# Optimization experiments

Measured on AMD Instinct MI355X. Metric: run time of the kernel, lower is better.

The kernel has to match this reference:

```python
import jax, jax.numpy as jnp
import numpy as np

B, C, L = 32, 512, 4096
H, K = 8, 3            # heads, kernel_size
D = C // H             # head dim
G = 32                 # GroupNorm groups
PAD = (K - 1) // 2
EPS = 1e-5
NEG = -1e30


def setup_inputs() -> dict:
    key = jax.random.key(0)
    ks = jax.random.split(key, 7)
    s = 0.02
    return {
        "x": jax.random.normal(ks[0], (B, C, L), dtype=jnp.float32),
        "gamma": jnp.ones((C,), dtype=jnp.float32),
        "beta": jnp.zeros((C,), dtype=jnp.float32),
        "W_k": jax.random.normal(ks[1], (C, H * D), dtype=jnp.float32) * s,
        "W_v": jax.random.normal(ks[2], (C, H * D), dtype=jnp.float32) * s,
        "W_o": jax.random.normal(ks[3], (H * D, C), dtype=jnp.float32) * s,
        "q": jax.random.normal(ks[4], (H, D), dtype=jnp.float32) * s,     # learned queries (QnA)
        "rpe": jax.random.normal(ks[5], (H, K), dtype=jnp.float32) * s,   # relative-position bias
    }


def _group_norm(x, gamma, beta):
    # x: (B, C, L); normalize over (C//G, L) within each of G groups
    b, c, l = x.shape
    xg = x.reshape(b, G, (c // G) * l)
    mu = jnp.mean(xg, axis=-1, keepdims=True)
    var = jnp.var(xg, axis=-1, keepdims=True)
    xn = ((xg - mu) * jax.lax.rsqrt(var + EPS)).reshape(b, c, l)
    return xn * gamma[None, :, None] + beta[None, :, None]


def reference(x, gamma, beta, W_k, W_v, W_o, q, rpe):
    h = _group_norm(x, gamma, beta)                     # (B, C, L)
    ht = jnp.transpose(h, (0, 2, 1))                    # (B, L, C)
    k = (ht @ W_k).reshape(B, L, H, D)                  # (B, L, H, D)
    v = (ht @ W_v).reshape(B, L, H, D)

    scale = 1.0 / np.sqrt(D).astype(np.float32)
    logits = jnp.einsum('blhd,hd->blh', k, q) * scale   # (B, L, H)

    # sliding windows of size K (zero-padded; -inf logits at boundaries)
    lp = jnp.pad(logits, ((0, 0), (PAD, PAD), (0, 0)), constant_values=NEG)
    lwin = jnp.stack([lp[:, j:j + L] for j in range(K)], axis=2)      # (B, L, K, H)
    lwin = lwin + jnp.transpose(rpe)[None, None]                       # rpe: (H,K)->(K,H)
    attn = jax.nn.softmax(lwin, axis=2)                                # (B, L, K, H)

    vp = jnp.pad(v, ((0, 0), (PAD, PAD), (0, 0), (0, 0)))
    vwin = jnp.stack([vp[:, j:j + L] for j in range(K)], axis=2)       # (B, L, K, H, D)
    o = jnp.einsum('blkh,blkhd->blhd', attn, vwin).reshape(B, L, H * D)

    out = (o @ W_o)                                      # (B, L, C)
    return x + jnp.transpose(out, (0, 2, 1))             # residual, (B, C, L)
```

## Files before the change

### kernel.cpp

```cpp
#include <hip/hip_runtime.h>

#define Bb 32
#define Cc 512
#define Ll 4096
#define Hh 8
#define Dd 64
#define Gg 32
#define BLt (Bb * Ll)
#define NKV 520
#define NKVPAD 640

typedef __attribute__((ext_vector_type(4))) float f32x4;
typedef __attribute__((ext_vector_type(8))) short short8;
typedef __attribute__((ext_vector_type(4))) short s16x4;
typedef __attribute__((ext_vector_type(4))) int int4v;

union U16 { int4v v; short s[8]; };

__device__ __forceinline__ float bf2f(short s) {
    unsigned u = ((unsigned)(unsigned short)s) << 16;
    float f; __builtin_memcpy(&f, &u, 4); return f;
}
__device__ __forceinline__ short f2bf(float f) {
    unsigned u; __builtin_memcpy(&u, &f, 4);
    u = (u + 0x7FFFu + ((u >> 16) & 1u)) >> 16;
    return (short)u;
}

__device__ __forceinline__ int kpack(int k) {
    int blk = k >> 5, r = k & 31;
    return blk * 32 + ((r & 15) >> 2) * 8 + ((r >> 4) << 2) + (r & 3);
}

__device__ __forceinline__ int swz_off(int row, int inner) {
    return row * 128 + (inner ^ ((row & 7) << 4));
}

__device__ __forceinline__ void gload16(const short* g, short* l) {
    __builtin_amdgcn_global_load_lds((const __attribute__((address_space(1))) unsigned int*)g,
                                     (__attribute__((address_space(3))) unsigned int*)l,
                                     16, 0, 0);
}
__device__ __forceinline__ void gload16f(const float* g, float* l) {
    __builtin_amdgcn_global_load_lds((const __attribute__((address_space(1))) unsigned int*)g,
                                     (__attribute__((address_space(3))) unsigned int*)l,
                                     16, 0, 0);
}

#define BAR() __builtin_amdgcn_s_barrier()
#define SFENCE() __builtin_amdgcn_sched_barrier(0)

__global__ void k_prep(const float* __restrict__ Wk, const float* __restrict__ Wv,
                       const float* __restrict__ Wo, const float* __restrict__ q,
                       short* __restrict__ Wct, short* __restrict__ Wot, int packWo)
{
    int bid = blockIdx.x, t = threadIdx.x;
    if (bid < NKVPAD) {
        int n = bid;
        if (n < 512) {
            for (int k = t; k < 512; k += 64)
                Wct[n * 512 + kpack(k)] = f2bf(Wv[k * 512 + n]);
        } else if (n < NKV) {
            int h = n - 512;
            for (int k = t; k < 512; k += 64) {
                float acc = 0.f;
                for (int d = 0; d < 64; ++d)
                    acc += Wk[k * 512 + h * 64 + d] * q[h * 64 + d];
                Wct[n * 512 + kpack(k)] = f2bf(acc * 0.125f);
            }
        } else {
            for (int k = t; k < 512; k += 64) Wct[n * 512 + kpack(k)] = 0;
        }
    } else {
        int c = bid - NKVPAD;
        for (int k = t; k < 512; k += 64)
            Wot[c * 512 + (packWo ? kpack(k) : k)] = f2bf(Wo[k * 512 + c]);
    }
}

__global__ void k_stats(const float* __restrict__ x, float* __restrict__ stats)
{
    int bg = blockIdx.x;
    const float* p = x + (size_t)bg * 65536;
    int t = threadIdx.x;
    float s = 0.f, ss = 0.f;
    for (int i = t * 4; i < 65536; i += 1024) {
        f32x4 v = *(const f32x4*)(p + i);
        s  += v[0] + v[1] + v[2] + v[3];
        ss += v[0]*v[0] + v[1]*v[1] + v[2]*v[2] + v[3]*v[3];
    }
    for (int o = 32; o > 0; o >>= 1) { s += __shfl_down(s, o); ss += __shfl_down(ss, o); }
    __shared__ float red[8];
    int lane = t & 63, w = t >> 6;
    if (lane == 0) { red[w] = s; red[4 + w] = ss; }
    __syncthreads();
    if (t == 0) {
        float S  = red[0] + red[1] + red[2] + red[3];
        float SS = red[4] + red[5] + red[6] + red[7];
        float mean = S * (1.0f / 65536.0f);
        float var  = SS * (1.0f / 65536.0f) - mean * mean;
        stats[bg * 2]     = mean;
        stats[bg * 2 + 1] = rsqrtf(var + 1e-5f);
    }
}

__global__ void k_norm_t(const float* __restrict__ x, const float* __restrict__ gamma,
                         const float* __restrict__ beta, const float* __restrict__ stats,
                         short* __restrict__ hT)
{
    __shared__ float tile[64 * 65];
    int b = blockIdx.z, c0 = blockIdx.y * 64, l0 = blockIdx.x * 64;
    int t = threadIdx.x;
    int lq = t & 15, cq = t >> 4;
    #pragma unroll
    for (int p = 0; p < 4; ++p) {
        int cl = cq + p * 16;
        int c = c0 + cl;
        float mean = stats[(b * 32 + (c >> 4)) * 2];
        float rstd = stats[(b * 32 + (c >> 4)) * 2 + 1];
        float a  = rstd * gamma[c];
        float bb = beta[c] - mean * a;
        f32x4 v = *(const f32x4*)(x + ((size_t)b << 21) + ((size_t)c << 12) + l0 + lq * 4);
        #pragma unroll
        for (int j = 0; j < 4; ++j) tile[cl * 65 + lq * 4 + j] = v[j] * a + bb;
    }
    __syncthreads();
    int ll = t >> 2, cq4 = t & 3;
    int bl = b * Ll + l0 + ll;
    short hbuf[16];
    #pragma unroll
    for (int j = 0; j < 16; ++j) hbuf[j] = f2bf(tile[(cq4 * 16 + j) * 65 + ll]);
    short* dst = hT + (size_t)bl * 512 + ((c0 >> 5) + (cq4 >> 1)) * 32 + ((cq4 & 1) << 2);
    #pragma unroll
    for (int jj = 0; jj < 4; ++jj) {
        s16x4 v4 = { hbuf[jj*4+0], hbuf[jj*4+1], hbuf[jj*4+2], hbuf[jj*4+3] };
        *(s16x4*)(dst + jj * 8) = v4;
    }
}

__launch_bounds__(256, 2)
__global__ void k_gemm1f(const short* __restrict__ A, const short* __restrict__ Bw,
                         short* __restrict__ vbuf, short* __restrict__ lbuf)
{
    __shared__ short sA[2][8192];
    __shared__ short sB[2][8192];
    __shared__ short wqlds[8192];
    const int t = threadIdx.x;
    const int nwg = 1024;
    const int bid = blockIdx.x;
    const int work = (bid & 7) * (nwg >> 3) + (bid >> 3);
    const int ntile = work & 3;
    const int n0 = ntile * 128;
    const int mbase = (work >> 2) * 512;

    const int lane = t & 63, wid = t >> 6;
    const int wm = wid >> 1, wn = wid & 1;
    const int g = lane >> 4, ln = lane & 15;

    {
        int row = t >> 5;
        int cp = (t & 31) * 2;
        int4v v0 = *(const int4v*)(Bw + (size_t)(512 + row) * 512 + cp * 8);
        int4v v1 = *(const int4v*)(Bw + (size_t)(512 + row) * 512 + cp * 8 + 8);
        *(int4v*)((char*)wqlds + row * 1024 + ((cp * 16) ^ ((row & 7) << 4))) = v0;
        *(int4v*)((char*)wqlds + row * 1024 + (((cp + 1) * 16) ^ ((row & 7) << 4))) = v1;
        int4v z = {0, 0, 0, 0};
        int row2 = 8 + (t >> 5);
        *(int4v*)((char*)wqlds + row2 * 1024 + ((cp * 16) ^ ((row2 & 7) << 4))) = z;
        *(int4v*)((char*)wqlds + row2 * 1024 + (((cp + 1) * 16) ^ ((row2 & 7) << 4))) = z;
    }
    asm volatile("s_waitcnt vmcnt(0) lgkmcnt(0)" ::: "memory");
    BAR(); SFENCE();

    const int srow = wid * 8 + (lane >> 3);
    const int sinner = (((lane & 7) ^ ((lane >> 3) & 7)) << 3);
    const short* gAs = A  + (size_t)(mbase + srow) * 512 + sinner;
    const short* gBs = Bw + (size_t)(n0 + srow) * 512 + sinner;

    f32x4 acc[4][4] = {};
    f32x4 accq[4] = {};

    auto stage = [&](int kt, int buf) {
        size_t offA = (size_t)(kt >> 3) * 65536 + (size_t)(kt & 7) * 64;
        size_t offB = (size_t)(kt & 7) * 64;
        #pragma unroll
        for (int gq = 0; gq < 4; ++gq) {
            gload16(gAs + (size_t)gq * 32 * 512 + offA, &sA[buf][gq * 2048 + wid * 512]);
            gload16(gBs + (size_t)gq * 32 * 512 + offB, &sB[buf][gq * 2048 + wid * 512]);
        }
    };
    auto compute = [&](int buf, int kk) {
        #pragma unroll
        for (int ks = 0; ks < 2; ++ks) {
            short8 af[4], bfr[4], bq;
            #pragma unroll
            for (int i = 0; i < 4; ++i) {
                af[i]  = *(const short8*)((const char*)&sA[buf][0] + swz_off(wm * 64 + i * 16 + ln, ks * 64 + g * 16));
                bfr[i] = *(const short8*)((const char*)&sB[buf][0] + swz_off(wn * 64 + i * 16 + ln, ks * 64 + g * 16));
            }
            bq = *(const short8*)((const char*)wqlds + ln * 1024 +
                                  ((kk * 128 + ks * 64 + g * 16) ^ ((ln & 7) << 4)));
            #pragma unroll
            for (int mi = 0; mi < 4; ++mi)
                #pragma unroll
                for (int ni = 0; ni < 4; ++ni)
                    acc[mi][ni] = __builtin_amdgcn_mfma_f32_16x16x32_bf16(af[mi], bfr[ni], acc[mi][ni], 0, 0, 0);
            #pragma unroll
            for (int mi = 0; mi < 4; ++mi)
                accq[mi] = __builtin_amdgcn_mfma_f32_16x16x32_bf16(af[mi], bq, accq[mi], 0, 0, 0);
        }
    };

    stage(0, 0); stage(1, 1);
    #pragma unroll 1
    for (int s = 0; s < 32; ++s) {
        if (s == 31)           asm volatile("s_waitcnt vmcnt(0)"  ::: "memory");
        else if ((s & 7) == 0 && s) asm volatile("s_waitcnt vmcnt(16)" ::: "memory");
        else                   asm volatile("s_waitcnt vmcnt(8)"  ::: "memory");
        BAR(); SFENCE();
        compute(s & 1, s & 7);
        SFENCE();
        if ((s & 7) == 7) {
            BAR();
            int m0 = mbase + (s >> 3) * 128;
            {
                short* scrW = &sB[s & 1][0] + wid * 2048;
                const int blkq = (lane & 7) >> 2, jq = lane & 3;
                #pragma unroll
                for (int p = 0; p < 2; ++p) {
                    #pragma unroll
                    for (int mh = 0; mh < 2; ++mh)
                        #pragma unroll
                        for (int ni = 0; ni < 4; ++ni)
                            #pragma unroll
                            for (int i = 0; i < 4; ++i)
                                scrW[(mh * 16 + g * 4 + i) * 64 + ni * 16 + ln] = f2bf(acc[p * 2 + mh][ni][i]);
                    asm volatile("s_waitcnt lgkmcnt(0)" ::: "memory"); SFENCE();
                    #pragma unroll
                    for (int it = 0; it < 4; ++it) {
                        int mrl = it * 8 + (lane >> 3);
                        const short* bp = scrW + mrl * 64 + blkq * 32;
                        s16x4 lo = *(const s16x4*)(bp + 4 * jq);
                        s16x4 hi = *(const s16x4*)(bp + 16 + 4 * jq);
                        union { int4v v; s16x4 h[2]; } ov;
                        ov.h[0] = lo; ov.h[1] = hi;
                        int m = m0 + wm * 64 + p * 32 + mrl;
                        int nc = n0 + wn * 64 + blkq * 32 + jq * 8;
                        *(int4v*)(vbuf + (size_t)m * 512 + nc) = ov.v;
                    }
                    asm volatile("s_waitcnt lgkmcnt(0)" ::: "memory"); SFENCE();
                }
            }
            if (ntile == 0 && wn == 0 && ln < 8) {
                #pragma unroll
                for (int mi = 0; mi < 4; ++mi)
                    #pragma unroll
                    for (int i = 0; i < 4; ++i) {
                        int m = m0 + wm * 64 + mi * 16 + g * 4 + i;
                        lbuf[(size_t)m * 8 + ln] = f2bf(accq[mi][i]);
                    }
            }
            #pragma unroll
            for (int mi = 0; mi < 4; ++mi) {
                #pragma unroll
                for (int ni = 0; ni < 4; ++ni)
                    acc[mi][ni] = (f32x4){0.f, 0.f, 0.f, 0.f};
                accq[mi] = (f32x4){0.f, 0.f, 0.f, 0.f};
            }
        }
        if (s < 30) { BAR(); stage(s + 2, s & 1); SFENCE(); }
    }
}

__global__ void k_attnw2(const short* __restrict__ lbuf, const float* __restrict__ rpe,
                         float* __restrict__ attnW)
{
    int tid = blockIdx.x * 256 + threadIdx.x;
    int bl = tid >> 3, h = tid & 7;
    int l = bl & (Ll - 1);
    float lg0 = (l > 0)      ? bf2f(lbuf[(size_t)(bl - 1) * 8 + h]) + rpe[h * 3 + 0] : -1e30f;
    float lg1 =                bf2f(lbuf[(size_t)bl * 8 + h])       + rpe[h * 3 + 1];
    float lg2 = (l < Ll - 1) ? bf2f(lbuf[(size_t)(bl + 1) * 8 + h]) + rpe[h * 3 + 2] : -1e30f;
    float m = fmaxf(lg1, fmaxf(lg0, lg2));
    float e0 = (l > 0)      ? __expf(lg0 - m) : 0.f;
    float e1 =                __expf(lg1 - m);
    float e2 = (l < Ll - 1) ? __expf(lg2 - m) : 0.f;
    float inv = 1.0f / (e0 + e1 + e2);
    f32x4 w = { e0 * inv, e1 * inv, e2 * inv, 0.0f };
    *(f32x4*)(attnW + (size_t)bl * 32 + h * 4) = w;
}

__launch_bounds__(256, 2)
__global__ void k_gemm2f(const short* __restrict__ Wot, const short* __restrict__ vbuf,
                         const float* __restrict__ attnW, const float* __restrict__ x,
                         float* __restrict__ out)
{
    __shared__ short sA[2][8192];
    __shared__ short sBc[2][8192];
    __shared__ float wlds[4096];
    const int t = threadIdx.x;
    const int nwg = 1024;
    const int bid = blockIdx.x;
    const int work = (bid & 7) * (nwg >> 3) + (bid >> 3);
    const int n0 = work * 128;

    const int lane = t & 63, wid = t >> 6;
    const int wm = wid >> 1, wn = wid & 1;
    const int g = lane >> 4, ln = lane & 15;

    const int srow = wid * 8 + (lane >> 3);
    const int sinner = (((lane & 7) ^ ((lane >> 3) & 7)) << 3);
    const short* gAs = Wot + (size_t)srow * 512 + sinner;

    unsigned ovm[4], ov0[4], ovp[4];
    #pragma unroll
    for (int q2 = 0; q2 < 4; ++q2) {
        int r = n0 + srow + 32 * q2;
        int l = r & (Ll - 1);
        int rm = (l == 0) ? r : r - 1;
        int rp = (l == Ll - 1) ? r : r + 1;
        ov0[q2] = (unsigned)r  * 1024u + (unsigned)sinner * 2u;
        ovm[q2] = (unsigned)rm * 1024u + (unsigned)sinner * 2u;
        ovp[q2] = (unsigned)rp * 1024u + (unsigned)sinner * 2u;
    }
    const char* vb = (const char*)vbuf;

    const int r4 = lane >> 4, lcm = (lane & 15) * 4;
    const int ngE = n0 + wn * 64 + lcm;
    const size_t rowbase = ((size_t)(ngE >> 12) << 21) + (size_t)(ngE & (Ll - 1));
    const float* xrow = x + rowbase;
    float* outrow = out + rowbase;

    f32x4 acc[4][4] = {};
    U16 Rm[4], R0[4], Rp[4];

    auto stageA = [&](int s, int buf) {
        size_t off = (size_t)(s >> 3) * 65536 + (size_t)(s & 7) * 64;
        #pragma unroll
        for (int gq = 0; gq < 4; ++gq)
            gload16(gAs + (size_t)gq * 32 * 512 + off, &sA[buf][gq * 2048 + wid * 512]);
    };
    auto loadR = [&](int s1) {
        unsigned off = (unsigned)(s1 & 7) * 128u;
        #pragma unroll
        for (int q2 = 0; q2 < 4; ++q2) {
            Rm[q2].v = *(const int4v*)(vb + ovm[q2] + off);
            R0[q2].v = *(const int4v*)(vb + ov0[q2] + off);
            Rp[q2].v = *(const int4v*)(vb + ovp[q2] + off);
        }
    };
    auto combineStep = [&](int s1, int buf) {
        int h = s1 & 7;
        #pragma unroll
        for (int q2 = 0; q2 < 4; ++q2) {
            int r = srow + 32 * q2;
            f32x4 w = *(const f32x4*)&wlds[r * 32 + ((h ^ (r & 7)) << 2)];
            U16 cm;
            #pragma unroll
            for (int j = 0; j < 8; ++j) {
                float o = w[0] * bf2f(Rm[q2].s[j]) + w[1] * bf2f(R0[q2].s[j])
                        + w[2] * bf2f(Rp[q2].s[j]);
                cm.s[j] = f2bf(o);
            }
            *(int4v*)((char*)&sBc[buf][0] + q2 * 4096 + wid * 1024 + lane * 16) = cm.v;
        }
    };
    auto compute = [&](int buf) {
        #pragma unroll
        for (int ks = 0; ks < 2; ++ks) {
            short8 af[4], bfr[4];
            #pragma unroll
            for (int i = 0; i < 4; ++i) {
                af[i]  = *(const short8*)((const char*)&sA[buf][0] + swz_off(wm * 64 + i * 16 + ln, ks * 64 + g * 16));
                bfr[i] = *(const short8*)((const char*)&sBc[buf][0] + swz_off(wn * 64 + i * 16 + ln, ks * 64 + g * 16));
            }
            #pragma unroll
            for (int mi = 0; mi < 4; ++mi)
                #pragma unroll
                for (int ni = 0; ni < 4; ++ni)
                    acc[mi][ni] = __builtin_amdgcn_mfma_f32_16x16x32_bf16(af[mi], bfr[ni], acc[mi][ni], 0, 0, 0);
        }
    };
    auto epilogue = [&](int s) {
        BAR();
        float* scr = (float*)((char*)&sA[s & 1][0] + wid * 4096);
        int m0c = (s >> 3) * 128;
        #pragma unroll
        for (int p = 0; p < 4; ++p) {
            #pragma unroll
            for (int ni = 0; ni < 4; ++ni)
                #pragma unroll
                for (int i = 0; i < 4; ++i) {
                    int r = g * 4 + i;
                    int col = (ni * 16 + ln) ^ ((((r & 3) ^ (r >> 2)) & 3) << 4);
                    scr[r * 64 + col] = acc[p][ni][i];
                }
            asm volatile("s_waitcnt lgkmcnt(0)" ::: "memory"); SFENCE();
            #pragma unroll
            for (int j = 0; j < 4; ++j) {
                int rr = r4 + 4 * j;
                int cst = lcm ^ ((((rr & 3) ^ (rr >> 2)) & 3) << 4);
                f32x4 sv = *(const f32x4*)&scr[rr * 64 + cst];
                int c = m0c + wm * 64 + p * 16 + rr;
                f32x4 xv = *(const f32x4*)(xrow + ((size_t)c << 12));
                *(f32x4*)(outrow + ((size_t)c << 12)) = xv + sv;
            }
            asm volatile("s_waitcnt lgkmcnt(0)" ::: "memory"); SFENCE();
        }
        #pragma unroll
        for (int mi = 0; mi < 4; ++mi)
            #pragma unroll
            for (int ni = 0; ni < 4; ++ni)
                acc[mi][ni] = (f32x4){0.f, 0.f, 0.f, 0.f};
    };

    stageA(0, 0); stageA(1, 1);
    {
        const float* wsrc = attnW + (size_t)n0 * 32;
        int rr = lane >> 3, hl = lane & 7;
        #pragma unroll
        for (int j = 0; j < 4; ++j) {
            int row = (wid * 4 + j) * 8 + rr;
            gload16f(wsrc + row * 32 + ((hl ^ (row & 7)) << 2), &wlds[(wid * 4 + j) * 256]);
        }
    }
    loadR(0); SFENCE();
    asm volatile("s_waitcnt vmcnt(0)" ::: "memory");
    BAR(); SFENCE();
    combineStep(0, 0);
    asm volatile("s_waitcnt lgkmcnt(0)" ::: "memory"); SFENCE();
    loadR(1); SFENCE();

    #pragma unroll 1
    for (int s = 0; s < 32; ++s) {
        if (s == 0 || s == 31)       asm volatile("s_waitcnt vmcnt(0)"  ::: "memory");
        else if ((s & 7) == 0)       asm volatile("s_waitcnt vmcnt(36)" ::: "memory");
        else                         asm volatile("s_waitcnt vmcnt(4)"  ::: "memory");
        BAR(); SFENCE();
        if (s < 31) {
            combineStep(s + 1, (s + 1) & 1);
            SFENCE();
            if (s < 30) { loadR(s + 2); SFENCE(); }
        }
        compute(s & 1);
        asm volatile("s_waitcnt lgkmcnt(0)" ::: "memory"); SFENCE();
        if ((s & 7) == 7) epilogue(s);
        if (s < 30) { BAR(); stageA(s + 2, s & 1); SFENCE(); }
    }
}

__launch_bounds__(256, 2)
__global__ void k_gemm1_fb(const short* __restrict__ A, const short* __restrict__ Bw,
                           short* __restrict__ kv)
{
    __shared__ short sA[2][8192];
    __shared__ short sB[2][8192];
    const int t = threadIdx.x;
    const int m0 = blockIdx.y * 128;
    const int n0 = blockIdx.x * 128;
    const int lane = t & 63, wid = t >> 6;
    const int wm = wid >> 1, wn = wid & 1;
    const int g = lane >> 4, ln = lane & 15;

    const int srow = wid * 8 + (lane >> 3);
    const int sinner = (((lane & 7) ^ ((lane >> 3) & 7)) << 3);
    const short* gAs = A  + (size_t)(m0 + srow) * 512 + sinner;
    const short* gBs = Bw + (size_t)(n0 + srow) * 512 + sinner;

    f32x4 acc[4][4] = {};

    auto stage = [&](int kt, int buf) {
        #pragma unroll
        for (int gq = 0; gq < 4; ++gq) {
            gload16(gAs + (size_t)gq * 32 * 512 + kt * 64, &sA[buf][gq * 2048 + wid * 512]);
            gload16(gBs + (size_t)gq * 32 * 512 + kt * 64, &sB[buf][gq * 2048 + wid * 512]);
        }
    };
    auto compute = [&](int buf) {
        #pragma unroll
        for (int ks = 0; ks < 2; ++ks) {
            short8 af[4], bfr[4];
            #pragma unroll
            for (int i = 0; i < 4; ++i) {
                af[i]  = *(const short8*)((const char*)&sA[buf][0] + swz_off(wm * 64 + i * 16 + ln, ks * 64 + g * 16));
                bfr[i] = *(const short8*)((const char*)&sB[buf][0] + swz_off(wn * 64 + i * 16 + ln, ks * 64 + g * 16));
            }
            #pragma unroll
            for (int mi = 0; mi < 4; ++mi)
                #pragma unroll
                for (int ni = 0; ni < 4; ++ni)
                    acc[mi][ni] = __builtin_amdgcn_mfma_f32_16x16x32_bf16(af[mi], bfr[ni], acc[mi][ni], 0, 0, 0);
        }
    };

    stage(0, 0);
    __syncthreads();
    #pragma unroll 1
    for (int kt = 0; kt < 8; ++kt) {
        if (kt < 7) stage(kt + 1, (kt + 1) & 1);
        compute(kt & 1);
        __syncthreads();
    }

    #pragma unroll
    for (int mi = 0; mi < 4; ++mi)
        #pragma unroll
        for (int ni = 0; ni < 4; ++ni) {
            int n = n0 + wn * 64 + ni * 16 + ln;
            if (n < NKV) {
                #pragma unroll
                for (int i = 0; i < 4; ++i) {
                    int m = m0 + wm * 64 + mi * 16 + g * 4 + i;
                    kv[(size_t)m * NKV + n] = f2bf(acc[mi][ni][i]);
                }
            }
        }
}

__global__ void k_attnw(const short* __restrict__ kv, const float* __restrict__ rpe,
                        float* __restrict__ attnW)
{
    int tid = blockIdx.x * 256 + threadIdx.x;
    int bl = tid >> 3, h = tid & 7;
    int l = bl & (Ll - 1);
    float lg[3];
    #pragma unroll
    for (int j = 0; j < 3; ++j) {
        bool valid = (j == 1) || (j == 0 && l > 0) || (j == 2 && l < Ll - 1);
        lg[j] = valid ? (bf2f(kv[(size_t)(bl + j - 1) * NKV + 512 + h]) + rpe[h * 3 + j])
                      : -1e30f;
    }
    float m = fmaxf(lg[0], fmaxf(lg[1], lg[2]));
    float e0 = __expf(lg[0] - m), e1 = __expf(lg[1] - m), e2 = __expf(lg[2] - m);
    float inv = 1.0f / (e0 + e1 + e2);
    f32x4 w = { e0 * inv, e1 * inv, e2 * inv, 0.0f };
    *(f32x4*)(attnW + (size_t)bl * 32 + h * 4) = w;
}

__launch_bounds__(256, 2)
__global__ void k_gemm2_fused(const short* __restrict__ Wot, const short* __restrict__ kv,
                              const float* __restrict__ attnW, const float* __restrict__ x,
                              float* __restrict__ out)
{
    __shared__ short sA[2][8192];
    __shared__ short sB[2][8192];
    const int t = threadIdx.x;
    const int m0 = blockIdx.x * 128;
    const int n0 = blockIdx.y * 128;
    const int lane = t & 63, wid = t >> 6;
    const int wm = wid >> 1, wn = wid & 1;
    const int g = lane >> 4, ln = lane & 15;
    const int sr = t >> 1, ksh = t & 1;

    const short* gA = Wot + (size_t)(m0 + sr) * 512 + ksh * 32;
    const int nrow = n0 + sr;
    const int lpos = nrow & (Ll - 1);
    const int nm1 = (lpos == 0) ? nrow : nrow - 1;
    const int np1 = (lpos == Ll - 1) ? nrow : nrow + 1;
    const short* gV0 = kv + (size_t)nrow * NKV + ksh * 32;
    const short* gVm = kv + (size_t)nm1  * NKV + ksh * 32;
    const short* gVp = kv + (size_t)np1  * NKV + ksh * 32;
    const float* gW = attnW + (size_t)nrow * 32;

    f32x4 acc[4][4] = {};
    U16 ra[4], rbm[4], rb0[4], rbp[4];
    f32x4 wv;

    auto load_tile = [&](int kt) {
        #pragma unroll
        for (int qq = 0; qq < 4; ++qq) {
            ra[qq].v  = *(const int4v*)(gA  + kt * 64 + qq * 8);
            rbm[qq].v = *(const int4v*)(gVm + kt * 64 + qq * 8);
            rb0[qq].v = *(const int4v*)(gV0 + kt * 64 + qq * 8);
            rbp[qq].v = *(const int4v*)(gVp + kt * 64 + qq * 8);
        }
        wv = *(const f32x4*)(gW + kt * 4);
    };
    auto write_tile = [&](int buf) {
        short ob[32];
        #pragma unroll
        for (int qq = 0; qq < 4; ++qq)
            #pragma unroll
            for (int j = 0; j < 8; ++j) {
                float o = wv[0] * bf2f(rbm[qq].s[j]) + wv[1] * bf2f(rb0[qq].s[j])
                        + wv[2] * bf2f(rbp[qq].s[j]);
                ob[qq * 8 + j] = f2bf(o);
            }
        #pragma unroll
        for (int f = 0; f < 4; ++f) {
            U16 wa, wb;
            #pragma unroll
            for (int j = 0; j < 4; ++j) {
                wa.s[j]     = ra[f >> 1].s[(f & 1) * 4 + j];
                wa.s[4 + j] = ra[2 + (f >> 1)].s[(f & 1) * 4 + j];
                wb.s[j]     = ob[4 * f + j];
                wb.s[4 + j] = ob[16 + 4 * f + j];
            }
            int off = swz_off(sr, ksh * 64 + f * 16);
            *(int4v*)((char*)&sA[buf][0] + off) = wa.v;
            *(int4v*)((char*)&sB[buf][0] + off) = wb.v;
        }
    };
    auto compute = [&](int buf) {
        #pragma unroll
        for (int ks = 0; ks < 2; ++ks) {
            short8 af[4], bfr[4];
            #pragma unroll
            for (int i = 0; i < 4; ++i) {
                af[i]  = *(const short8*)((const char*)&sA[buf][0] + swz_off(wm * 64 + i * 16 + ln, ks * 64 + g * 16));
                bfr[i] = *(const short8*)((const char*)&sB[buf][0] + swz_off(wn * 64 + i * 16 + ln, ks * 64 + g * 16));
            }
            #pragma unroll
            for (int mi = 0; mi < 4; ++mi)
                #pragma unroll
                for (int ni = 0; ni < 4; ++ni)
                    acc[mi][ni] = __builtin_amdgcn_mfma_f32_16x16x32_bf16(af[mi], bfr[ni], acc[mi][ni], 0, 0, 0);
        }
    };

    load_tile(0); write_tile(0); __syncthreads();
    #pragma unroll 1
    for (int kt = 0; kt < 8; ++kt) {
        if (kt < 7) load_tile(kt + 1);
        compute(kt & 1);
        if (kt < 7) write_tile((kt + 1) & 1);
        __syncthreads();
    }

    #pragma unroll
    for (int mi = 0; mi < 4; ++mi)
        #pragma unroll
        for (int ni = 0; ni < 4; ++ni)
            #pragma unroll
            for (int i = 0; i < 4; ++i) {
                int c = m0 + wm * 64 + mi * 16 + g * 4 + i;
                int ng = n0 + wn * 64 + ni * 16 + ln;
                int b = ng >> 12, l = ng & (Ll - 1);
                size_t off = ((size_t)b << 21) | ((size_t)c << 12) | (size_t)l;
                out[off] = x[off] + acc[mi][ni][i];
            }
}

extern "C" void kernel_launch(void* const* d_in, const int* in_sizes, int n_in,
                              void* d_out, int out_size, void* d_ws, size_t ws_size,
                              hipStream_t stream)
{
    const float* x     = (const float*)d_in[0];
    const float* gamma = (const float*)d_in[1];
    const float* beta  = (const float*)d_in[2];
    const float* Wk    = (const float*)d_in[3];
    const float* Wv    = (const float*)d_in[4];
    const float* Wo    = (const float*)d_in[5];
    const float* q     = (const float*)d_in[6];
    const float* rpe   = (const float*)d_in[7];
    float* out = (float*)d_out;
    char* ws = (char*)d_ws;

    const size_t MB128 = 134217728ull;
    const size_t MAIN_WS = MB128 * 2 + 655360 + 524288 + 2097152 + 8192;

    if (ws_size >= MAIN_WS) {
        float* attnW = (float*)(ws);
        short* vbuf  = (short*)(ws + MB128);
        short* Wct   = (short*)(ws + 2 * MB128);
        short* Wot   = (short*)(ws + 2 * MB128 + 655360);
        short* lbuf  = (short*)(ws + 2 * MB128 + 655360 + 524288);
        float* stats = (float*)(ws + 2 * MB128 + 655360 + 524288 + 2097152);
        short* hT    = (short*)d_out;

        k_prep<<<1152, 64, 0, stream>>>(Wk, Wv, Wo, q, Wct, Wot, 1);
        k_stats<<<1024, 256, 0, stream>>>(x, stats);
        k_norm_t<<<dim3(64, 8, 32), 256, 0, stream>>>(x, gamma, beta, stats, hT);
        k_gemm1f<<<1024, 256, 0, stream>>>(hT, Wct, vbuf, lbuf);
        k_attnw2<<<4096, 256, 0, stream>>>(lbuf, rpe, attnW);
        k_gemm2f<<<1024, 256, 0, stream>>>(Wot, vbuf, attnW, x, out);
    } else {
        short* Wct   = (short*)(ws + 0);
        short* Wot   = (short*)(ws + 655360);
        float* stats = (float*)(ws + 1179648);
        float* attnW = (float*)(ws + 1187840);
        short* kv    = (short*)(ws + 17965056);
        short* hT    = (short*)d_out;

        k_prep<<<1152, 64, 0, stream>>>(Wk, Wv, Wo, q, Wct, Wot, 0);
        k_stats<<<1024, 256, 0, stream>>>(x, stats);
        k_norm_t<<<dim3(64, 8, 32), 256, 0, stream>>>(x, gamma, beta, stats, hT);
        k_gemm1_fb<<<dim3(5, 1024), 256, 0, stream>>>(hT, Wct, kv);
        k_attnw<<<4096, 256, 0, stream>>>(kv, rpe, attnW);
        k_gemm2_fused<<<dim3(4, 1024), 256, 0, stream>>>(Wot, kv, attnW, x, out);
    }
}
```

Measured before the change: 509.8 us.

## Stage V tiles into LDS once and combine sliding window from shared memory

Replaces the per-thread loads of three neighbouring V rows (previous, current, next) from global memory with a single async global-to-LDS staging of each V tile. The tile goes into a triple-buffered LDS array, and the window combine reads the neighbour rows from LDS. Only the two tile-boundary halo rows are fetched separately from global memory. The attention weights are now loaded directly from global memory per step instead of being staged in LDS. This removes the threefold redundant global V traffic, but it adds an extra barrier inside the combine step and keeps the existing vmcnt wait counts, which were tuned for the old load mix.

```diff
diff --git a/kernel.cpp b/kernel.cpp
--- a/kernel.cpp
+++ b/kernel.cpp
@@ -37,11 +37,6 @@
 }
 
 __device__ __forceinline__ void gload16(const short* g, short* l) {
-    __builtin_amdgcn_global_load_lds((const __attribute__((address_space(1))) unsigned int*)g,
-                                     (__attribute__((address_space(3))) unsigned int*)l,
-                                     16, 0, 0);
-}
-__device__ __forceinline__ void gload16f(const float* g, float* l) {
     __builtin_amdgcn_global_load_lds((const __attribute__((address_space(1))) unsigned int*)g,
                                      (__attribute__((address_space(3))) unsigned int*)l,
                                      16, 0, 0);
@@ -296,8 +291,7 @@
                          float* __restrict__ out)
 {
     __shared__ short sA[2][8192];
-    __shared__ short sBc[2][8192];
-    __shared__ float wlds[4096];
+    __shared__ short rawV[3][8192];
     const int t = threadIdx.x;
     const int nwg = 1024;
     const int bid = blockIdx.x;
@@ -309,21 +303,21 @@
     const int g = lane >> 4, ln = lane & 15;
 
     const int srow = wid * 8 + (lane >> 3);
-    const int sinner = (((lane & 7) ^ ((lane >> 3) & 7)) << 3);
-    const short* gAs = Wot + (size_t)srow * 512 + sinner;
-
-    unsigned ovm[4], ov0[4], ovp[4];
-    #pragma unroll
-    for (int q2 = 0; q2 < 4; ++q2) {
-        int r = n0 + srow + 32 * q2;
-        int l = r & (Ll - 1);
-        int rm = (l == 0) ? r : r - 1;
-        int rp = (l == Ll - 1) ? r : r + 1;
-        ov0[q2] = (unsigned)r  * 1024u + (unsigned)sinner * 2u;
-        ovm[q2] = (unsigned)rm * 1024u + (unsigned)sinner * 2u;
-        ovp[q2] = (unsigned)rp * 1024u + (unsigned)sinner * 2u;
-    }
-    const char* vb = (const char*)vbuf;
+    const int gch = lane & 7;
+    const int sinner = ((gch ^ (srow & 7)) << 3);
+    const short* gAs = Wot  + (size_t)srow * 512 + sinner;
+    const short* gVs = vbuf + (size_t)(n0 + srow) * 512 + sinner;
+
+    const int s_own = (gch ^ (srow & 7)) << 4;
+    const int s_rm  = (gch ^ ((srow - 1) & 7)) << 4;
+    const int s_rp  = (gch ^ ((srow + 1) & 7)) << 4;
+
+    const int rbnd = (srow == 0) ? ((n0 == 0) ? 0 : n0 - 1)
+                   : ((srow == 31) ? ((n0 + 128 >= BLt) ? BLt - 1 : n0 + 128)
+                                   : n0 + srow);
+    const short* gBnd = vbuf + (size_t)rbnd * 512 + gch * 8;
+
+    const float* gW = attnW + (size_t)(n0 + srow) * 32;
 
     const int r4 = lane >> 4, lcm = (lane & 15) * 4;
     const int ngE = n0 + wn * 64 + lcm;
@@ -332,7 +326,8 @@
     float* outrow = out + rowbase;
 
     f32x4 acc[4][4] = {};
-    U16 Rm[4], R0[4], Rp[4];
+    f32x4 wq[4];
+    U16 bnd;
 
     auto stageA = [&](int s, int buf) {
         size_t off = (size_t)(s >> 3) * 65536 + (size_t)(s & 7) * 64;
@@ -340,39 +335,57 @@
         for (int gq = 0; gq < 4; ++gq)
             gload16(gAs + (size_t)gq * 32 * 512 + off, &sA[buf][gq * 2048 + wid * 512]);
     };
-    auto loadR = [&](int s1) {
-        unsigned off = (unsigned)(s1 & 7) * 128u;
-        #pragma unroll
-        for (int q2 = 0; q2 < 4; ++q2) {
-            Rm[q2].v = *(const int4v*)(vb + ovm[q2] + off);
-            R0[q2].v = *(const int4v*)(vb + ov0[q2] + off);
-            Rp[q2].v = *(const int4v*)(vb + ovp[q2] + off);
-        }
-    };
-    auto combineStep = [&](int s1, int buf) {
+    auto stageV = [&](int s1) {
+        int b = s1 % 3;
+        size_t off = (size_t)(s1 & 7) * 64;
+        #pragma unroll
+        for (int gq = 0; gq < 4; ++gq)
+            gload16(gVs + (size_t)gq * 32 * 512 + off, &rawV[b][gq * 2048 + wid * 512]);
+    };
+    auto loadWB = [&](int s1) {
         int h = s1 & 7;
+        #pragma unroll
+        for (int q2 = 0; q2 < 4; ++q2)
+            wq[q2] = *(const f32x4*)(gW + q2 * 32 * 32 + h * 4);
+        bnd.v = *(const int4v*)(gBnd + (size_t)h * 64);
+    };
+    auto combine = [&](int s1) {
+        int b = s1 % 3;
+        const char* base = (const char*)&rawV[b][0];
+        U16 vm[4], v0[4], vp[4];
         #pragma unroll
         for (int q2 = 0; q2 < 4; ++q2) {
             int r = srow + 32 * q2;
-            f32x4 w = *(const f32x4*)&wlds[r * 32 + ((h ^ (r & 7)) << 2)];
+            v0[q2].v = *(const int4v*)(base + r * 128 + s_own);
+            vm[q2].v = *(const int4v*)(base + ((r - 1) & 127) * 128 + s_rm);
+            vp[q2].v = *(const int4v*)(base + ((r + 1) & 127) * 128 + s_rp);
+        }
+        asm volatile("s_waitcnt lgkmcnt(0)" ::: "memory"); SFENCE();
+        if (srow == 0)  vm[0] = bnd;
+        if (srow == 31) vp[3] = bnd;
+        BAR(); SFENCE();
+        char* wbase = (char*)&rawV[b][0];
+        #pragma unroll
+        for (int q2 = 0; q2 < 4; ++q2) {
+            int r = srow + 32 * q2;
             U16 cm;
             #pragma unroll
             for (int j = 0; j < 8; ++j) {
-                float o = w[0] * bf2f(Rm[q2].s[j]) + w[1] * bf2f(R0[q2].s[j])
-                        + w[2] * bf2f(Rp[q2].s[j]);
+                float o = wq[q2][0] * bf2f(vm[q2].s[j]) + wq[q2][1] * bf2f(v0[q2].s[j])
+                        + wq[q2][2] * bf2f(vp[q2].s[j]);
                 cm.s[j] = f2bf(o);
             }
-            *(int4v*)((char*)&sBc[buf][0] + q2 * 4096 + wid * 1024 + lane * 16) = cm.v;
-        }
-    };
-    auto compute = [&](int buf) {
+            *(int4v*)(wbase + r * 128 + s_own) = cm.v;
+        }
+    };
+    auto compute = [&](int vb3, int ab) {
         #pragma unroll
         for (int ks = 0; ks < 2; ++ks) {
             short8 af[4], bfr[4];
             #pragma unroll
             for (int i = 0; i < 4; ++i) {
-                af[i]  = *(const short8*)((const char*)&sA[buf][0] + swz_off(wm * 64 + i * 16 + ln, ks * 64 + g * 16));
-                bfr[i] = *(const short8*)((const char*)&sBc[buf][0] + swz_off(wn * 64 + i * 16 + ln, ks * 64 + g * 16));
+                af[i]  = *(const short8*)((const char*)&sA[ab][0] + swz_off(wm * 64 + i * 16 + ln, ks * 64 + g * 16));
+                bfr[i] = *(const short8*)((const char*)&rawV[vb3][0] + swz_off(wn * 64 + i * 16 + ln, ks * 64 + g * 16));
             }
             #pragma unroll
             for (int mi = 0; mi < 4; ++mi)
@@ -415,34 +428,27 @@
     };
 
     stageA(0, 0); stageA(1, 1);
-    {
-        const float* wsrc = attnW + (size_t)n0 * 32;
-        int rr = lane >> 3, hl = lane & 7;
-        #pragma unroll
-        for (int j = 0; j < 4; ++j) {
-            int row = (wid * 4 + j) * 8 + rr;
-            gload16f(wsrc + row * 32 + ((hl ^ (row & 7)) << 2), &wlds[(wid * 4 + j) * 256]);
-        }
-    }
-    loadR(0); SFENCE();
+    stageV(0); stageV(1);
+    loadWB(0); SFENCE();
     asm volatile("s_waitcnt vmcnt(0)" ::: "memory");
     BAR(); SFENCE();
-    combineStep(0, 0);
+    combine(0);
     asm volatile("s_waitcnt lgkmcnt(0)" ::: "memory"); SFENCE();
-    loadR(1); SFENCE();
+    loadWB(1); SFENCE();
 
     #pragma unroll 1
     for (int s = 0; s < 32; ++s) {
-        if (s == 0 || s == 31)       asm volatile("s_waitcnt vmcnt(0)"  ::: "memory");
-        else if ((s & 7) == 0)       asm volatile("s_waitcnt vmcnt(36)" ::: "memory");
-        else                         asm volatile("s_waitcnt vmcnt(4)"  ::: "memory");
+        if (s == 0 || s == 31)  asm volatile("s_waitcnt vmcnt(0)"  ::: "memory");
+        else if ((s & 7) == 0)  asm volatile("s_waitcnt vmcnt(36)" ::: "memory");
+        else                    asm volatile("s_waitcnt vmcnt(4)"  ::: "memory");
         BAR(); SFENCE();
+        if (s < 30) { stageV(s + 2); SFENCE(); }
         if (s < 31) {
-            combineStep(s + 1, (s + 1) & 1);
+            combine(s + 1);
             SFENCE();
-            if (s < 30) { loadR(s + 2); SFENCE(); }
-        }
-        compute(s & 1);
+            if (s < 30) { loadWB(s + 2); SFENCE(); }
+        }
+        compute(s % 3, s & 1);
         asm volatile("s_waitcnt lgkmcnt(0)" ::: "memory"); SFENCE();
         if ((s & 7) == 7) epilogue(s);
         if (s < 30) { BAR(); stageA(s + 2, s & 1); SFENCE(); }
```

After: 528.5 us. 3.7% more time.
